# Kernel optimization log

Hardware: AMD Instinct MI355X
Metric: run time of the kernel (lower is better)

The kernel has to match this reference:

```python
import jax, jax.numpy as jnp
import numpy as np

GRID_SIZE = 3
SPLINE_ORDER = 3
N_BASIS = GRID_SIZE + SPLINE_ORDER  # 6


def make_grid(in_features, dtype=jnp.float32):
    # efficient-kan grid buffer: extended uniform knots over grid_range=[-1, 1]
    h = 2.0 / GRID_SIZE
    g = jnp.arange(-SPLINE_ORDER, GRID_SIZE + SPLINE_ORDER + 1, dtype=dtype) * h - 1.0
    return jnp.tile(g[None, :], (in_features, 1))  # (in, G + 2S + 1)


def b_splines(x, grid):
    # x: (N, in), grid: (in, G+2S+1) -> (N, in, G+S) via Cox-de Boor recursion
    xb = x[..., None]
    bases = ((xb >= grid[:, :-1]) & (xb < grid[:, 1:])).astype(x.dtype)
    for k in range(1, SPLINE_ORDER + 1):
        bases = ((xb - grid[:, : -(k + 1)]) / (grid[:, k:-1] - grid[:, : -(k + 1)]) * bases[..., :-1]
                 + (grid[:, k + 1:] - xb) / (grid[:, k + 1:] - grid[:, 1:-k]) * bases[..., 1:])
    return bases


def kan_linear(x, base_w, spline_w, scaler, grid):
    # base path: silu(x) @ W_base^T ; spline path: contraction of basis with scaled spline weights
    base = jax.nn.silu(x) @ base_w.T
    scaled_sw = spline_w * scaler[..., None]  # (out, in, K)
    spl = jnp.einsum('nik,oik->no', b_splines(x, grid), scaled_sw)
    return base + spl


def setup_inputs() -> dict:
    key = jax.random.key(0)
    ks = jax.random.split(key, 7)
    B, C, P, D, H = 8, 8, 128, 256, 1024
    s = 0.05
    return {
        'x': jax.random.normal(ks[0], (B, C, P, D), dtype=jnp.float32),
        'base_w1': s * jax.random.normal(ks[1], (H, D), dtype=jnp.float32),
        'spline_w1': s * jax.random.normal(ks[2], (H, D, N_BASIS), dtype=jnp.float32),
        'scaler1': 1.0 + s * jax.random.normal(ks[3], (H, D), dtype=jnp.float32),
        'base_w2': s * jax.random.normal(ks[4], (D, H), dtype=jnp.float32),
        'spline_w2': s * jax.random.normal(ks[5], (D, H, N_BASIS), dtype=jnp.float32),
        'scaler2': 1.0 + s * jax.random.normal(ks[6], (D, H), dtype=jnp.float32),
    }


def reference(x, base_w1, spline_w1, scaler1, base_w2, spline_w2, scaler2):
    B, C, P, D = x.shape
    H = base_w1.shape[0]
    xf = x.reshape(-1, D)  # KANLinear flattens leading dims to tokens
    g1 = make_grid(D, x.dtype)
    g2 = make_grid(H, x.dtype)
    h = kan_linear(xf, base_w1, spline_w1, scaler1, g1)
    h = jax.nn.gelu(h, approximate=False)  # torch F.gelu default = exact erf
    # dropout is identity in eval / with p used as inference baseline
    y = kan_linear(h, base_w2, spline_w2, scaler2, g2)
    return y.reshape(B, C, P, D)
```

## Files before the change

### kernel.cpp

```cpp
#include <hip/hip_runtime.h>
#include <hip/hip_bf16.h>
#include <math.h>


typedef __attribute__((ext_vector_type(8))) short bf16x8;
typedef __attribute__((ext_vector_type(4))) float f32x4;

#define TOKENS 8192
#define D_IN   256
#define D_HID  1024

__device__ __forceinline__ void kan_features(float x, float f[8]) {
    f[0] = x * __builtin_amdgcn_rcpf(1.0f + __expf(-x));
    const float s = (x + 1.0f) * 1.5f + 3.0f;
    const float cf = floorf(s);
    const float u = s - cf;
    const int c = (int)cf;
    const float u2 = u * u, u3 = u2 * u;
    const float k6 = 1.0f / 6.0f;
    const float v3 = u3 * k6;
    const float v2 = (-3.0f * u3 + 3.0f * u2 + 3.0f * u + 1.0f) * k6;
    const float v1 = (3.0f * u3 - 6.0f * u2 + 4.0f) * k6;
    const float w1 = 1.0f - u;
    const float v0 = w1 * w1 * w1 * k6;
    const bool in = (s >= 0.0f) && (s < 9.0f);
#pragma unroll
    for (int j = 0; j < 6; ++j) {
        int d = c - j;
        float bv = (d == 0) ? v3 : (d == 1) ? v2 : (d == 2) ? v1 : (d == 3) ? v0 : 0.0f;
        f[1 + j] = in ? bv : 0.0f;
    }
    f[7] = 0.0f;
}

__device__ __forceinline__ void features_to_bf16(const float f[8], __hip_bfloat16 fb[8]) {
#pragma unroll
    for (int j = 0; j < 8; ++j) fb[j] = __float2bfloat16(f[j]);
}

__global__ void prep_weights(const float* __restrict__ bw,
                             const float* __restrict__ sw,
                             const float* __restrict__ sc,
                             __hip_bfloat16* __restrict__ Waug, int total) {
    int idx = blockIdx.x * blockDim.x + threadIdx.x;
    if (idx >= total) return;
    float scl = sc[idx];
    __hip_bfloat16 row[8];
    row[0] = __float2bfloat16(bw[idx]);
#pragma unroll
    for (int j = 0; j < 6; ++j)
        row[1 + j] = __float2bfloat16(sw[idx * 6 + j] * scl);
    row[7] = __float2bfloat16(0.0f);
    *(bf16x8*)&Waug[(size_t)idx * 8] = *(bf16x8*)row;
}

__global__ void expand_x(const float* __restrict__ X, __hip_bfloat16* __restrict__ F,
                         int total) {
    int idx = blockIdx.x * blockDim.x + threadIdx.x;
    if (idx >= total) return;
    float f[8];
    kan_features(X[idx], f);
    __hip_bfloat16 fb[8];
    features_to_bf16(f, fb);
    *(bf16x8*)&F[(size_t)idx * 8] = *(bf16x8*)fb;
}

#define GLL(src, dst) __builtin_amdgcn_global_load_lds(                         \
    (const __attribute__((address_space(1))) void*)(src),                       \
    (__attribute__((address_space(3))) void*)(dst), 16, 0, 0)

__global__ __launch_bounds__(256, 2)
void kan_gemm1(const __hip_bfloat16* __restrict__ A,
               const __hip_bfloat16* __restrict__ W,
               float* __restrict__ H) {
    constexpr int K = D_IN * 8;
    constexpr int NT = K / 64;
    __shared__ __hip_bfloat16 Al[2][128 * 64];
    __shared__ __hip_bfloat16 Bl[2][128 * 64];

    const int tid = threadIdx.x;
    const int wid = tid >> 6, lane = tid & 63;
    const int wm = wid >> 1, wn = wid & 1;
    const int lr = lane & 15, lg = lane >> 4;
    const int n0 = blockIdx.x * 128, o0 = blockIdx.y * 128;

    int srow[4], sslot[4];
#pragma unroll
    for (int p = 0; p < 4; ++p) {
        int item = tid + p * 256;
        srow[p] = item >> 3;
        sslot[p] = (item & 7) ^ (srow[p] & 7);
    }
    int aoff[2][4], boff[2][4];
#pragma unroll
    for (int ks = 0; ks < 2; ++ks)
#pragma unroll
        for (int f = 0; f < 4; ++f) {
            int ar = wm * 64 + f * 16 + lr;
            int br = wn * 64 + f * 16 + lr;
            aoff[ks][f] = ar * 64 + (((ks * 4 + lg) ^ (ar & 7)) * 8);
            boff[ks][f] = br * 64 + (((ks * 4 + lg) ^ (br & 7)) * 8);
        }

    f32x4 acc[4][4] = {};

#define STG1(buf, kt)                                                           \
    do {                                                                        \
        _Pragma("unroll")                                                       \
        for (int p = 0; p < 4; ++p) {                                           \
            GLL(A + (size_t)(n0 + srow[p]) * K + (kt) * 64 + sslot[p] * 8,      \
                &Al[buf][(tid + p * 256) * 8]);                                 \
            GLL(W + (size_t)(o0 + srow[p]) * K + (kt) * 64 + sslot[p] * 8,      \
                &Bl[buf][(tid + p * 256) * 8]);                                 \
        }                                                                       \
    } while (0)

    STG1(0, 0);
    STG1(1, 1);
    for (int t = 0; t < NT; ++t) {
        const int cur = t & 1;
        asm volatile("s_waitcnt vmcnt(8)" ::: "memory");
        __builtin_amdgcn_s_barrier();
        __builtin_amdgcn_sched_barrier(0);
#pragma unroll
        for (int ks = 0; ks < 2; ++ks) {
            bf16x8 af[4], bfr[4];
#pragma unroll
            for (int f = 0; f < 4; ++f) af[f] = *(const bf16x8*)&Al[cur][aoff[ks][f]];
#pragma unroll
            for (int f = 0; f < 4; ++f) bfr[f] = *(const bf16x8*)&Bl[cur][boff[ks][f]];
#pragma unroll
            for (int fm = 0; fm < 4; ++fm)
#pragma unroll
                for (int fn = 0; fn < 4; ++fn)
                    acc[fm][fn] = __builtin_amdgcn_mfma_f32_16x16x32_bf16(
                        af[fm], bfr[fn], acc[fm][fn], 0, 0, 0);
        }
        asm volatile("s_waitcnt lgkmcnt(0)" ::: "memory");
        __builtin_amdgcn_s_barrier();
        __builtin_amdgcn_sched_barrier(0);
        const int kn = (t + 2 < NT) ? t + 2 : NT - 1;
        STG1(cur, kn);
    }
#undef STG1
#pragma unroll
    for (int fm = 0; fm < 4; ++fm) {
#pragma unroll
        for (int fn = 0; fn < 4; ++fn) {
            int col = o0 + wn * 64 + fn * 16 + lr;
#pragma unroll
            for (int r = 0; r < 4; ++r) {
                int row = n0 + wm * 64 + fm * 16 + lg * 4 + r;
                float v = acc[fm][fn][r];
                H[(size_t)row * D_HID + col] = 0.5f * v * (1.0f + erff(v * 0.70710678118f));
            }
        }
    }
}

__global__ __launch_bounds__(256, 4)
void kan_gemm2(const float* __restrict__ H,
               const __hip_bfloat16* __restrict__ W,
               float* __restrict__ P) {
    constexpr int OUT = D_IN, KD = D_HID * 8;
    constexpr int NTT = KD / 64;
    __shared__ __hip_bfloat16 Al[64 * 64];
    __shared__ __hip_bfloat16 Bl[256 * 64];

    const int tid = threadIdx.x;
    const int wid = tid >> 6, lane = tid & 63;
    const int lr = lane & 15, lg = lane >> 4;
    const int n0 = blockIdx.x * 64;

    const int per = NTT / 8;
    const int ks0 = blockIdx.z * per, ks1 = ks0 + per;

    int srow[8], sslot[8];
#pragma unroll
    for (int p = 0; p < 8; ++p) {
        int item = tid + p * 256;
        srow[p] = item >> 3;
        sslot[p] = (item & 7) ^ (srow[p] & 7);
    }
    const int ar0 = tid >> 3, ac = tid & 7;
    const float* hp0 = H + (size_t)(n0 + ar0) * D_HID + ac;
    const float* hp1 = H + (size_t)(n0 + ar0 + 32) * D_HID + ac;
    const int aw0 = ar0 * 64 + ((ac ^ (ar0 & 7)) * 8);
    const int aw1 = (ar0 + 32) * 64 + ((ac ^ (ar0 & 7)) * 8);

    int aoff[2][4], boff[2][4];
#pragma unroll
    for (int ks = 0; ks < 2; ++ks)
#pragma unroll
        for (int f = 0; f < 4; ++f) {
            int ar = f * 16 + lr;
            int br = wid * 64 + f * 16 + lr;
            aoff[ks][f] = ar * 64 + (((ks * 4 + lg) ^ (ar & 7)) * 8);
            boff[ks][f] = br * 64 + (((ks * 4 + lg) ^ (br & 7)) * 8);
        }

    f32x4 acc[4][4] = {};

    float hv0 = hp0[(size_t)ks0 * 8];
    float hv1 = hp1[(size_t)ks0 * 8];

    for (int kt = ks0; kt < ks1; ++kt) {
        float hc0 = hv0, hc1 = hv1;
        const int knext = (kt + 1 < ks1) ? kt + 1 : ks1 - 1;
        hv0 = hp0[(size_t)knext * 8];
        hv1 = hp1[(size_t)knext * 8];
        {
            float ff[8]; __hip_bfloat16 fb[8];
            kan_features(hc0, ff); features_to_bf16(ff, fb);
            *(bf16x8*)&Al[aw0] = *(bf16x8*)fb;
            kan_features(hc1, ff); features_to_bf16(ff, fb);
            *(bf16x8*)&Al[aw1] = *(bf16x8*)fb;
        }
#pragma unroll
        for (int p = 0; p < 8; ++p)
            GLL(W + (size_t)srow[p] * KD + (size_t)kt * 64 + sslot[p] * 8,
                &Bl[(tid + p * 256) * 8]);
        __syncthreads();
#pragma unroll
        for (int ks = 0; ks < 2; ++ks) {
            bf16x8 af[4], bfr[4];
#pragma unroll
            for (int f = 0; f < 4; ++f) af[f] = *(const bf16x8*)&Al[aoff[ks][f]];
#pragma unroll
            for (int f = 0; f < 4; ++f) bfr[f] = *(const bf16x8*)&Bl[boff[ks][f]];
#pragma unroll
            for (int fm = 0; fm < 4; ++fm)
#pragma unroll
                for (int fn = 0; fn < 4; ++fn)
                    acc[fm][fn] = __builtin_amdgcn_mfma_f32_16x16x32_bf16(
                        af[fm], bfr[fn], acc[fm][fn], 0, 0, 0);
        }
        __syncthreads();
    }

    float* Pl = (float*)Bl;
    const size_t zoff = (size_t)blockIdx.z * TOKENS * OUT;
#pragma unroll
    for (int h = 0; h < 2; ++h) {
        __syncthreads();
        if ((wid >> 1) == h) {
#pragma unroll
            for (int fm = 0; fm < 4; ++fm)
#pragma unroll
                for (int fn = 0; fn < 4; ++fn) {
                    int c = (wid & 1) * 64 + fn * 16 + lr;
#pragma unroll
                    for (int r = 0; r < 4; ++r)
                        Pl[(fm * 16 + lg * 4 + r) * 128 + c] = acc[fm][fn][r];
                }
        }
        __syncthreads();
#pragma unroll
        for (int q = 0; q < 8; ++q) {
            int v = tid + q * 256;
            int row = v >> 5, cv = (v & 31) * 4;
            *(f32x4*)&P[zoff + (size_t)(n0 + row) * OUT + h * 128 + cv] =
                *(const f32x4*)&Pl[row * 128 + cv];
        }
    }
}

__global__ void reduce_split(const float* __restrict__ P, float* __restrict__ out,
                             int nvec) {
    int i = blockIdx.x * 256 + threadIdx.x;
    if (i >= nvec) return;
    const f32x4* Pv = (const f32x4*)P;
    f32x4 s = Pv[i];
#pragma unroll
    for (int z = 1; z < 8; ++z) s += Pv[(size_t)z * nvec + i];
    ((f32x4*)out)[i] = s;
}

extern "C" void kernel_launch(void* const* d_in, const int* in_sizes, int n_in,
                              void* d_out, int out_size, void* d_ws, size_t ws_size,
                              hipStream_t stream) {
    const float* x   = (const float*)d_in[0];
    const float* bw1 = (const float*)d_in[1];
    const float* sw1 = (const float*)d_in[2];
    const float* sc1 = (const float*)d_in[3];
    const float* bw2 = (const float*)d_in[4];
    const float* sw2 = (const float*)d_in[5];
    const float* sc2 = (const float*)d_in[6];
    float* out = (float*)d_out;

    char* ws = (char*)d_ws;
    __hip_bfloat16* W1 = (__hip_bfloat16*)ws;
    __hip_bfloat16* W2 = (__hip_bfloat16*)(ws + (4ull << 20));
    __hip_bfloat16* F1 = (__hip_bfloat16*)(ws + (8ull << 20));
    float*          Hb = (float*)(ws + (40ull << 20));
    float*          Pp = (float*)(ws + (72ull << 20));

    if (ws_size < (136ull << 20)) return;

    const int totW = D_HID * D_IN;
    prep_weights<<<(totW + 255) / 256, 256, 0, stream>>>(bw1, sw1, sc1, W1, totW);
    prep_weights<<<(totW + 255) / 256, 256, 0, stream>>>(bw2, sw2, sc2, W2, totW);

    const int totX = TOKENS * D_IN;
    expand_x<<<(totX + 255) / 256, 256, 0, stream>>>(x, F1, totX);

    kan_gemm1<<<dim3(TOKENS / 128, D_HID / 128), 256, 0, stream>>>(F1, W1, Hb);

    kan_gemm2<<<dim3(TOKENS / 64, 1, 8), 256, 0, stream>>>(Hb, W2, Pp);

    const int nvec = TOKENS * D_IN / 4;
    reduce_split<<<(nvec + 255) / 256, 256, 0, stream>>>(Pp, out, nvec);
}
```

Measured before the change: 142.2 us.

## Fuse init kernels into one launch and halve gemm2 K-tile for occupancy

The three preprocessing kernels (two weight preps and the x feature expansion) are merged into a single launch that dispatches on block index. kan_gemm2's K-tile drops from 64 to 32, which halves shared memory per block and the per-thread H loads, and launch bounds rise to 5 blocks per CU. The epilogue now writes 64-column chunks one wave at a time. The aim is fewer launch gaps and higher occupancy in gemm2, paid for with twice as many loop iterations and barriers per block.

```diff
diff --git a/kernel.cpp b/kernel.cpp
--- a/kernel.cpp
+++ b/kernel.cpp
@@ -38,12 +38,27 @@
     for (int j = 0; j < 8; ++j) fb[j] = __float2bfloat16(f[j]);
 }
 
-__global__ void prep_weights(const float* __restrict__ bw,
-                             const float* __restrict__ sw,
-                             const float* __restrict__ sc,
-                             __hip_bfloat16* __restrict__ Waug, int total) {
-    int idx = blockIdx.x * blockDim.x + threadIdx.x;
-    if (idx >= total) return;
+__global__ void init_fused(const float* __restrict__ X, __hip_bfloat16* __restrict__ F,
+                           const float* __restrict__ bw1, const float* __restrict__ sw1,
+                           const float* __restrict__ sc1, __hip_bfloat16* __restrict__ W1,
+                           const float* __restrict__ bw2, const float* __restrict__ sw2,
+                           const float* __restrict__ sc2, __hip_bfloat16* __restrict__ W2) {
+    const int b = blockIdx.x;
+    if (b < 8192) {
+        int idx = b * 256 + threadIdx.x;
+        float f[8];
+        kan_features(X[idx], f);
+        __hip_bfloat16 fb[8];
+        features_to_bf16(f, fb);
+        *(bf16x8*)&F[(size_t)idx * 8] = *(bf16x8*)fb;
+        return;
+    }
+    const bool w1 = (b < 9216);
+    int idx = (w1 ? (b - 8192) : (b - 9216)) * 256 + threadIdx.x;
+    const float* bw = w1 ? bw1 : bw2;
+    const float* sw = w1 ? sw1 : sw2;
+    const float* sc = w1 ? sc1 : sc2;
+    __hip_bfloat16* Wo = w1 ? W1 : W2;
     float scl = sc[idx];
     __hip_bfloat16 row[8];
     row[0] = __float2bfloat16(bw[idx]);
@@ -51,18 +66,7 @@
     for (int j = 0; j < 6; ++j)
         row[1 + j] = __float2bfloat16(sw[idx * 6 + j] * scl);
     row[7] = __float2bfloat16(0.0f);
-    *(bf16x8*)&Waug[(size_t)idx * 8] = *(bf16x8*)row;
-}
-
-__global__ void expand_x(const float* __restrict__ X, __hip_bfloat16* __restrict__ F,
-                         int total) {
-    int idx = blockIdx.x * blockDim.x + threadIdx.x;
-    if (idx >= total) return;
-    float f[8];
-    kan_features(X[idx], f);
-    __hip_bfloat16 fb[8];
-    features_to_bf16(f, fb);
-    *(bf16x8*)&F[(size_t)idx * 8] = *(bf16x8*)fb;
+    *(bf16x8*)&Wo[(size_t)idx * 8] = *(bf16x8*)row;
 }
 
 #define GLL(src, dst) __builtin_amdgcn_global_load_lds(                         \
@@ -158,14 +162,14 @@
     }
 }
 
-__global__ __launch_bounds__(256, 4)
+__global__ __launch_bounds__(256, 5)
 void kan_gemm2(const float* __restrict__ H,
                const __hip_bfloat16* __restrict__ W,
                float* __restrict__ P) {
     constexpr int OUT = D_IN, KD = D_HID * 8;
-    constexpr int NTT = KD / 64;
-    __shared__ __hip_bfloat16 Al[64 * 64];
-    __shared__ __hip_bfloat16 Bl[256 * 64];
+    constexpr int NTT = KD / 32;
+    __shared__ __hip_bfloat16 Al[64 * 32];
+    __shared__ __hip_bfloat16 Bl[256 * 32];
 
     const int tid = threadIdx.x;
     const int wid = tid >> 6, lane = tid & 63;
@@ -175,92 +179,78 @@
     const int per = NTT / 8;
     const int ks0 = blockIdx.z * per, ks1 = ks0 + per;
 
-    int srow[8], sslot[8];
-#pragma unroll
-    for (int p = 0; p < 8; ++p) {
+    int srow[4], sslot[4];
+#pragma unroll
+    for (int p = 0; p < 4; ++p) {
         int item = tid + p * 256;
-        srow[p] = item >> 3;
-        sslot[p] = (item & 7) ^ (srow[p] & 7);
-    }
-    const int ar0 = tid >> 3, ac = tid & 7;
-    const float* hp0 = H + (size_t)(n0 + ar0) * D_HID + ac;
-    const float* hp1 = H + (size_t)(n0 + ar0 + 32) * D_HID + ac;
-    const int aw0 = ar0 * 64 + ((ac ^ (ar0 & 7)) * 8);
-    const int aw1 = (ar0 + 32) * 64 + ((ac ^ (ar0 & 7)) * 8);
-
-    int aoff[2][4], boff[2][4];
-#pragma unroll
-    for (int ks = 0; ks < 2; ++ks)
-#pragma unroll
-        for (int f = 0; f < 4; ++f) {
-            int ar = f * 16 + lr;
-            int br = wid * 64 + f * 16 + lr;
-            aoff[ks][f] = ar * 64 + (((ks * 4 + lg) ^ (ar & 7)) * 8);
-            boff[ks][f] = br * 64 + (((ks * 4 + lg) ^ (br & 7)) * 8);
-        }
+        srow[p] = item >> 2;
+        sslot[p] = (item & 3) ^ (srow[p] & 3);
+    }
+    const int frow = tid >> 2, fc = tid & 3;
+    const float* hp = H + (size_t)(n0 + frow) * D_HID + fc;
+    const int aw = frow * 32 + ((fc ^ (frow & 3)) * 8);
+
+    int aoff[4], boff[4];
+#pragma unroll
+    for (int f = 0; f < 4; ++f) {
+        int ar = f * 16 + lr;
+        int br = wid * 64 + f * 16 + lr;
+        aoff[f] = ar * 32 + ((lg ^ (ar & 3)) * 8);
+        boff[f] = br * 32 + ((lg ^ (br & 3)) * 8);
+    }
 
     f32x4 acc[4][4] = {};
 
-    float hv0 = hp0[(size_t)ks0 * 8];
-    float hv1 = hp1[(size_t)ks0 * 8];
-
+    float hv = hp[(size_t)ks0 * 4];
     for (int kt = ks0; kt < ks1; ++kt) {
-        float hc0 = hv0, hc1 = hv1;
+        float hc = hv;
         const int knext = (kt + 1 < ks1) ? kt + 1 : ks1 - 1;
-        hv0 = hp0[(size_t)knext * 8];
-        hv1 = hp1[(size_t)knext * 8];
+        hv = hp[(size_t)knext * 4];
         {
             float ff[8]; __hip_bfloat16 fb[8];
-            kan_features(hc0, ff); features_to_bf16(ff, fb);
-            *(bf16x8*)&Al[aw0] = *(bf16x8*)fb;
-            kan_features(hc1, ff); features_to_bf16(ff, fb);
-            *(bf16x8*)&Al[aw1] = *(bf16x8*)fb;
-        }
-#pragma unroll
-        for (int p = 0; p < 8; ++p)
-            GLL(W + (size_t)srow[p] * KD + (size_t)kt * 64 + sslot[p] * 8,
+            kan_features(hc, ff); features_to_bf16(ff, fb);
+            *(bf16x8*)&Al[aw] = *(bf16x8*)fb;
+        }
+#pragma unroll
+        for (int p = 0; p < 4; ++p)
+            GLL(W + (size_t)srow[p] * KD + (size_t)kt * 32 + sslot[p] * 8,
                 &Bl[(tid + p * 256) * 8]);
         __syncthreads();
-#pragma unroll
-        for (int ks = 0; ks < 2; ++ks) {
-            bf16x8 af[4], bfr[4];
-#pragma unroll
-            for (int f = 0; f < 4; ++f) af[f] = *(const bf16x8*)&Al[aoff[ks][f]];
-#pragma unroll
-            for (int f = 0; f < 4; ++f) bfr[f] = *(const bf16x8*)&Bl[boff[ks][f]];
-#pragma unroll
-            for (int fm = 0; fm < 4; ++fm)
-#pragma unroll
-                for (int fn = 0; fn < 4; ++fn)
-                    acc[fm][fn] = __builtin_amdgcn_mfma_f32_16x16x32_bf16(
-                        af[fm], bfr[fn], acc[fm][fn], 0, 0, 0);
-        }
+        bf16x8 af[4], bfr[4];
+#pragma unroll
+        for (int f = 0; f < 4; ++f) af[f] = *(const bf16x8*)&Al[aoff[f]];
+#pragma unroll
+        for (int f = 0; f < 4; ++f) bfr[f] = *(const bf16x8*)&Bl[boff[f]];
+#pragma unroll
+        for (int fm = 0; fm < 4; ++fm)
+#pragma unroll
+            for (int fn = 0; fn < 4; ++fn)
+                acc[fm][fn] = __builtin_amdgcn_mfma_f32_16x16x32_bf16(
+                    af[fm], bfr[fn], acc[fm][fn], 0, 0, 0);
         __syncthreads();
     }
 
     float* Pl = (float*)Bl;
     const size_t zoff = (size_t)blockIdx.z * TOKENS * OUT;
 #pragma unroll
-    for (int h = 0; h < 2; ++h) {
-        __syncthreads();
-        if ((wid >> 1) == h) {
+    for (int q = 0; q < 4; ++q) {
+        __syncthreads();
+        if (wid == q) {
 #pragma unroll
             for (int fm = 0; fm < 4; ++fm)
 #pragma unroll
-                for (int fn = 0; fn < 4; ++fn) {
-                    int c = (wid & 1) * 64 + fn * 16 + lr;
+                for (int fn = 0; fn < 4; ++fn)
 #pragma unroll
                     for (int r = 0; r < 4; ++r)
-                        Pl[(fm * 16 + lg * 4 + r) * 128 + c] = acc[fm][fn][r];
-                }
-        }
-        __syncthreads();
-#pragma unroll
-        for (int q = 0; q < 8; ++q) {
-            int v = tid + q * 256;
-            int row = v >> 5, cv = (v & 31) * 4;
-            *(f32x4*)&P[zoff + (size_t)(n0 + row) * OUT + h * 128 + cv] =
-                *(const f32x4*)&Pl[row * 128 + cv];
+                        Pl[(fm * 16 + lg * 4 + r) * 64 + fn * 16 + lr] = acc[fm][fn][r];
+        }
+        __syncthreads();
+#pragma unroll
+        for (int p = 0; p < 4; ++p) {
+            int v = tid + p * 256;
+            int row = v >> 4, cv = (v & 15) * 4;
+            *(f32x4*)&P[zoff + (size_t)(n0 + row) * OUT + q * 64 + cv] =
+                *(const f32x4*)&Pl[row * 64 + cv];
         }
     }
 }
@@ -297,12 +287,7 @@
 
     if (ws_size < (136ull << 20)) return;
 
-    const int totW = D_HID * D_IN;
-    prep_weights<<<(totW + 255) / 256, 256, 0, stream>>>(bw1, sw1, sc1, W1, totW);
-    prep_weights<<<(totW + 255) / 256, 256, 0, stream>>>(bw2, sw2, sc2, W2, totW);
-
-    const int totX = TOKENS * D_IN;
-    expand_x<<<(totX + 255) / 256, 256, 0, stream>>>(x, F1, totX);
+    init_fused<<<10240, 256, 0, stream>>>(x, F1, bw1, sw1, sc1, W1, bw2, sw2, sc2, W2);
 
     kan_gemm1<<<dim3(TOKENS / 128, D_HID / 128), 256, 0, stream>>>(F1, W1, Hb);
 
```

Result: slower. 152.9 us (+7.5%).

## Fuse prep kernels, fold split-K reduction into gemm2, add MFMA setprio

Applied to the files above, without the earlier changes.

Merges weight prep and input feature expansion into one launch. Replaces the separate split-K reduction kernel with a last-arriving-block reduction inside gemm2, using per-tile atomic counters that a memset clears beforehand. Wraps the MFMA loops in s_setprio to favour the compute waves. This cuts launch count and reduce-pass overhead, at the cost of an extra memset and threadfence/atomic synchronisation.

```diff
diff --git a/kernel.cpp b/kernel.cpp
--- a/kernel.cpp
+++ b/kernel.cpp
@@ -38,12 +38,27 @@
     for (int j = 0; j < 8; ++j) fb[j] = __float2bfloat16(f[j]);
 }
 
-__global__ void prep_weights(const float* __restrict__ bw,
-                             const float* __restrict__ sw,
-                             const float* __restrict__ sc,
-                             __hip_bfloat16* __restrict__ Waug, int total) {
-    int idx = blockIdx.x * blockDim.x + threadIdx.x;
-    if (idx >= total) return;
+__global__ void init_fused(const float* __restrict__ X, __hip_bfloat16* __restrict__ F,
+                           const float* __restrict__ bw1, const float* __restrict__ sw1,
+                           const float* __restrict__ sc1, __hip_bfloat16* __restrict__ W1,
+                           const float* __restrict__ bw2, const float* __restrict__ sw2,
+                           const float* __restrict__ sc2, __hip_bfloat16* __restrict__ W2) {
+    const int b = blockIdx.x;
+    if (b < 8192) {
+        int idx = b * 256 + threadIdx.x;
+        float f[8];
+        kan_features(X[idx], f);
+        __hip_bfloat16 fb[8];
+        features_to_bf16(f, fb);
+        *(bf16x8*)&F[(size_t)idx * 8] = *(bf16x8*)fb;
+        return;
+    }
+    const bool w1 = (b < 9216);
+    int idx = (w1 ? (b - 8192) : (b - 9216)) * 256 + threadIdx.x;
+    const float* bw = w1 ? bw1 : bw2;
+    const float* sw = w1 ? sw1 : sw2;
+    const float* sc = w1 ? sc1 : sc2;
+    __hip_bfloat16* Wo = w1 ? W1 : W2;
     float scl = sc[idx];
     __hip_bfloat16 row[8];
     row[0] = __float2bfloat16(bw[idx]);
@@ -51,18 +66,7 @@
     for (int j = 0; j < 6; ++j)
         row[1 + j] = __float2bfloat16(sw[idx * 6 + j] * scl);
     row[7] = __float2bfloat16(0.0f);
-    *(bf16x8*)&Waug[(size_t)idx * 8] = *(bf16x8*)row;
-}
-
-__global__ void expand_x(const float* __restrict__ X, __hip_bfloat16* __restrict__ F,
-                         int total) {
-    int idx = blockIdx.x * blockDim.x + threadIdx.x;
-    if (idx >= total) return;
-    float f[8];
-    kan_features(X[idx], f);
-    __hip_bfloat16 fb[8];
-    features_to_bf16(f, fb);
-    *(bf16x8*)&F[(size_t)idx * 8] = *(bf16x8*)fb;
+    *(bf16x8*)&Wo[(size_t)idx * 8] = *(bf16x8*)row;
 }
 
 #define GLL(src, dst) __builtin_amdgcn_global_load_lds(                         \
@@ -122,6 +126,7 @@
         asm volatile("s_waitcnt vmcnt(8)" ::: "memory");
         __builtin_amdgcn_s_barrier();
         __builtin_amdgcn_sched_barrier(0);
+        __builtin_amdgcn_s_setprio(1);
 #pragma unroll
         for (int ks = 0; ks < 2; ++ks) {
             bf16x8 af[4], bfr[4];
@@ -136,6 +141,7 @@
                     acc[fm][fn] = __builtin_amdgcn_mfma_f32_16x16x32_bf16(
                         af[fm], bfr[fn], acc[fm][fn], 0, 0, 0);
         }
+        __builtin_amdgcn_s_setprio(0);
         asm volatile("s_waitcnt lgkmcnt(0)" ::: "memory");
         __builtin_amdgcn_s_barrier();
         __builtin_amdgcn_sched_barrier(0);
@@ -161,11 +167,14 @@
 __global__ __launch_bounds__(256, 4)
 void kan_gemm2(const float* __restrict__ H,
                const __hip_bfloat16* __restrict__ W,
-               float* __restrict__ P) {
+               float* __restrict__ P,
+               float* __restrict__ out,
+               unsigned* __restrict__ counters) {
     constexpr int OUT = D_IN, KD = D_HID * 8;
     constexpr int NTT = KD / 64;
     __shared__ __hip_bfloat16 Al[64 * 64];
     __shared__ __hip_bfloat16 Bl[256 * 64];
+    __shared__ unsigned done_ct;
 
     const int tid = threadIdx.x;
     const int wid = tid >> 6, lane = tid & 63;
@@ -221,6 +230,7 @@
             GLL(W + (size_t)srow[p] * KD + (size_t)kt * 64 + sslot[p] * 8,
                 &Bl[(tid + p * 256) * 8]);
         __syncthreads();
+        __builtin_amdgcn_s_setprio(1);
 #pragma unroll
         for (int ks = 0; ks < 2; ++ks) {
             bf16x8 af[4], bfr[4];
@@ -235,6 +245,7 @@
                     acc[fm][fn] = __builtin_amdgcn_mfma_f32_16x16x32_bf16(
                         af[fm], bfr[fn], acc[fm][fn], 0, 0, 0);
         }
+        __builtin_amdgcn_s_setprio(0);
         __syncthreads();
     }
 
@@ -263,17 +274,26 @@
                 *(const f32x4*)&Pl[row * 128 + cv];
         }
     }
-}
-
-__global__ void reduce_split(const float* __restrict__ P, float* __restrict__ out,
-                             int nvec) {
-    int i = blockIdx.x * 256 + threadIdx.x;
-    if (i >= nvec) return;
-    const f32x4* Pv = (const f32x4*)P;
-    f32x4 s = Pv[i];
-#pragma unroll
-    for (int z = 1; z < 8; ++z) s += Pv[(size_t)z * nvec + i];
-    ((f32x4*)out)[i] = s;
+
+    __threadfence();
+    __syncthreads();
+    if (tid == 0) done_ct = atomicAdd(&counters[blockIdx.x], 1u);
+    __syncthreads();
+    if (done_ct == 7u) {
+        __threadfence();
+        constexpr int NV = 64 * OUT / 4;
+#pragma unroll
+        for (int p = 0; p < NV / 256; ++p) {
+            int v = tid + p * 256;
+            int row = v >> 6, cv = (v & 63) * 4;
+            const size_t off = (size_t)(n0 + row) * OUT + cv;
+            f32x4 s = *(const f32x4*)&P[off];
+#pragma unroll
+            for (int z = 1; z < 8; ++z)
+                s += *(const f32x4*)&P[(size_t)z * TOKENS * OUT + off];
+            *(f32x4*)&out[off] = s;
+        }
+    }
 }
 
 extern "C" void kernel_launch(void* const* d_in, const int* in_sizes, int n_in,
@@ -294,20 +314,15 @@
     __hip_bfloat16* F1 = (__hip_bfloat16*)(ws + (8ull << 20));
     float*          Hb = (float*)(ws + (40ull << 20));
     float*          Pp = (float*)(ws + (72ull << 20));
+    unsigned*       ct = (unsigned*)(ws + (8ull << 20));
 
     if (ws_size < (136ull << 20)) return;
 
-    const int totW = D_HID * D_IN;
-    prep_weights<<<(totW + 255) / 256, 256, 0, stream>>>(bw1, sw1, sc1, W1, totW);
-    prep_weights<<<(totW + 255) / 256, 256, 0, stream>>>(bw2, sw2, sc2, W2, totW);
-
-    const int totX = TOKENS * D_IN;
-    expand_x<<<(totX + 255) / 256, 256, 0, stream>>>(x, F1, totX);
+    init_fused<<<10240, 256, 0, stream>>>(x, F1, bw1, sw1, sc1, W1, bw2, sw2, sc2, W2);
 
     kan_gemm1<<<dim3(TOKENS / 128, D_HID / 128), 256, 0, stream>>>(F1, W1, Hb);
 
-    kan_gemm2<<<dim3(TOKENS / 64, 1, 8), 256, 0, stream>>>(Hb, W2, Pp);
-
-    const int nvec = TOKENS * D_IN / 4;
-    reduce_split<<<(nvec + 255) / 256, 256, 0, stream>>>(Pp, out, nvec);
-}
+    hipMemsetAsync(ct, 0, 128 * sizeof(unsigned), stream);
+
+    kan_gemm2<<<dim3(TOKENS / 64, 1, 8), 256, 0, stream>>>(Hb, W2, Pp, out, ct);
+}
```

New measurement: 285.5 us. +100.8%, slower.
